# Kernel optimization log

Hardware: AMD Instinct MI355X
Metric: run time of the kernel (lower is better)

The kernel has to match this reference:

```python
import jax, jax.numpy as jnp
import numpy as np

E, D, H, B = 8, 64, 512, 32768  # n_experts, state_dim, hidden width, batch
IN = D + 3  # x, t, sin(omega*t), cos(omega*t)


def setup_inputs() -> dict:
    key = jax.random.key(0)
    ks = jax.random.split(key, 12)
    s = 0.02
    return {
        "t": jax.random.uniform(ks[0], (1,), dtype=jnp.float32),
        "x": jax.random.normal(ks[1], (B, D), dtype=jnp.float32),
        "expert_weights": jax.random.uniform(ks[2], (B, E), dtype=jnp.float32),
        "omega": jnp.arange(1, E + 1, dtype=jnp.float32),  # omega_i = i+1
        "W1": jax.random.normal(ks[3], (E, H, IN), dtype=jnp.float32) * s,
        "b1": jnp.zeros((E, H), dtype=jnp.float32),
        "W2": jax.random.normal(ks[4], (E, H, H), dtype=jnp.float32) * s,
        "b2": jnp.zeros((E, H), dtype=jnp.float32),
        "W3": jax.random.normal(ks[5], (E, H, H), dtype=jnp.float32) * s,
        "b3": jnp.zeros((E, H), dtype=jnp.float32),
        "W4": jax.random.normal(ks[6], (E, D, H), dtype=jnp.float32) * s,
        "b4": jnp.zeros((E, D), dtype=jnp.float32),
    }


def reference(t, x, expert_weights, omega, W1, b1, W2, b2, W3, b3, W4, b4):
    # Dense path of ExpertODEEnsemble.forward: all experts active.
    nB = x.shape[0]
    tb = jnp.broadcast_to(t, (nB,))                       # (B,)
    wt = omega[:, None] * tb[None, :]                     # (E, B)
    # Per-expert inputs: [x, t, sin(wt), cos(wt)] -> (E, B, D+3)
    xe = jnp.broadcast_to(x[None], (E, nB, D))
    te = jnp.broadcast_to(tb[None, :, None], (E, nB, 1))
    inp = jnp.concatenate([xe, te, jnp.sin(wt)[..., None], jnp.cos(wt)[..., None]], axis=-1)
    h = jnp.tanh(jnp.einsum('ebi,ehi->ebh', inp, W1) + b1[:, None, :])
    h = jnp.tanh(jnp.einsum('ebh,egh->ebg', h, W2) + b2[:, None, :])
    h = jnp.tanh(jnp.einsum('ebh,egh->ebg', h, W3) + b3[:, None, :])
    dyn = jnp.einsum('ebh,edh->ebd', h, W4) + b4[:, None, :]   # (E, B, D)
    # Weighted combine: sum_e w[b,e] * dyn[e,b,:]
    dx_dt = jnp.einsum('be,ebd->bd', expert_weights, dyn)
    return dx_dt
```

## Files before the change

### kernel.cpp

```cpp
#include <hip/hip_runtime.h>
#include <hip/hip_bf16.h>


typedef unsigned short ushort_t;
typedef unsigned int u32;
typedef unsigned long long u64;
typedef __attribute__((ext_vector_type(8))) short short8;
typedef __attribute__((ext_vector_type(4))) float floatx4;
typedef __attribute__((ext_vector_type(16))) float floatx16;
typedef __attribute__((ext_vector_type(4))) int intx4;

#define W1A_OFF 0u
#define W2A_OFF 524288u
#define W3A_OFF 4718592u
#define W4A_OFF 8912896u
#define XB_OFF  9437184u
#define B1E_OFF 13631488u

#define SLOTB 16384
#define X_OFF_L 131072
#define SYNC_OFF 147456
#define SMEM_SZ 147552

static __device__ __forceinline__ u32 pk2bf(float a, float b) {
  union { __hip_bfloat162 h; u32 u; } v;
  v.h = __float22bfloat162_rn(make_float2(a, b));
  return v.u;
}

static __device__ __forceinline__ float pade_tanh(float x) {
  float x2 = x * x;
  float num = __builtin_fmaf(x2, __builtin_fmaf(x2, 1.0f, 105.0f), 945.0f);
  float den = __builtin_fmaf(x2, __builtin_fmaf(x2, 15.0f, 420.0f), 945.0f);
  return x * num * __builtin_amdgcn_rcpf(den);
}

static __device__ __forceinline__ void ald16(const void* g, void* l) {
  __builtin_amdgcn_global_load_lds((__attribute__((address_space(1))) void*)g,
                                   (__attribute__((address_space(3))) void*)l,
                                   16, 0, 0);
}

static __device__ __forceinline__ floatx16 mfma32(short8 a, short8 b, floatx16 c) {
  return __builtin_amdgcn_mfma_f32_32x32x16_bf16(a, b, c, 0, 0, 0);
}

static __device__ __forceinline__ int slot8(int g, int b) {
  return ((g + b) & 7) * SLOTB;
}

static __device__ __forceinline__ void waitge(const int* p, int tgt) {
  while (*(volatile const int*)p < tgt) __builtin_amdgcn_s_sleep(1);
  __asm__ __volatile__("" ::: "memory");
}

static __device__ __forceinline__ void waitge4(const int* p, int tgt) {
  for (;;) {
    __asm__ __volatile__("" ::: "memory");
    intx4 v = *(const intx4*)p;
    if (v[0] >= tgt && v[1] >= tgt && v[2] >= tgt && v[3] >= tgt) break;
    __builtin_amdgcn_s_sleep(1);
  }
  __asm__ __volatile__("" ::: "memory");
}

static __device__ __forceinline__ void guard_grp(const int* grp, int w, int base) {
  int tg0 = base + ((0 - w - 1) & 7) + 1;
  int tg1 = base + ((1 - w - 1) & 7) + 1;
  int tg2 = base + ((2 - w - 1) & 7) + 1;
  int tg3 = base + ((3 - w - 1) & 7) + 1;
  int tg4 = base + ((4 - w - 1) & 7) + 1;
  int tg5 = base + ((5 - w - 1) & 7) + 1;
  int tg6 = base + ((6 - w - 1) & 7) + 1;
  int tg7 = base + ((7 - w - 1) & 7) + 1;
  for (;;) {
    __asm__ __volatile__("" ::: "memory");
    intx4 a = *(const intx4*)grp;
    intx4 b = *(const intx4*)(grp + 4);
    if (a[0] >= tg0 && a[1] >= tg1 && a[2] >= tg2 && a[3] >= tg3 &&
        b[0] >= tg4 && b[1] >= tg5 && b[2] >= tg6 && b[3] >= tg7) break;
    __builtin_amdgcn_s_sleep(1);
  }
  __asm__ __volatile__("" ::: "memory");
}

static __device__ __forceinline__ void bump(int* p, int lane) {
  __asm__ __volatile__("s_waitcnt lgkmcnt(0)" ::: "memory");
  if (lane == 0) atomicAdd(p, 1);
}

static __device__ __forceinline__ void bump_sig(int* p, int lane) {
  __builtin_amdgcn_sched_barrier(0);
  if (lane == 0) atomicAdd(p, 1);
}

__global__ __launch_bounds__(256) void prep_kernel(
    const float* __restrict__ t, const float* __restrict__ x,
    const float* __restrict__ omega, const float* __restrict__ W1,
    const float* __restrict__ b1, const float* __restrict__ W2,
    const float* __restrict__ W3, const float* __restrict__ W4,
    char* __restrict__ ws) {
  int i = blockIdx.x * 256 + threadIdx.x;
  if (i < 32768) {
    int e = i >> 12, d = i & 4095;
    int lane = d & 63, q = d >> 6;
    int ol = q & 1, kc = (q >> 1) & 3, w = q >> 3;
    int outr = w * 64 + ol * 32 + (lane & 31);
    int kg = kc * 2 + (lane >> 5);
    const float* s = W1 + (e * 512 + outr) * 67 + kg * 8;
    ((intx4*)(ws + W1A_OFF))[i] = (intx4){
        (int)pk2bf(s[0], s[1]), (int)pk2bf(s[2], s[3]),
        (int)pk2bf(s[4], s[5]), (int)pk2bf(s[6], s[7])};
    return;
  }
  i -= 32768;
  if (i < 262144) {
    int e = i >> 15, d = i & 32767;
    int lane = d & 63, q = d >> 6;
    int ol = q & 1, kc = (q >> 1) & 31, w = q >> 6;
    int outr = w * 64 + ol * 32 + (lane & 31);
    int kg = kc * 2 + (lane >> 5);
    const floatx4* s = (const floatx4*)(W2 + ((e << 9) + outr) * 512 + (kg << 3));
    floatx4 lo = s[0], hi = s[1];
    ((intx4*)(ws + W2A_OFF))[i] = (intx4){
        (int)pk2bf(lo[0], lo[1]), (int)pk2bf(lo[2], lo[3]),
        (int)pk2bf(hi[0], hi[1]), (int)pk2bf(hi[2], hi[3])};
    return;
  }
  i -= 262144;
  if (i < 262144) {
    int e = i >> 15, d = i & 32767;
    int lane = d & 63, q = d >> 6;
    int ol = q & 1, kc = (q >> 1) & 31, w = q >> 6;
    int outr = w * 64 + ol * 32 + (lane & 31);
    int kg = kc * 2 + (lane >> 5);
    const floatx4* s = (const floatx4*)(W3 + ((e << 9) + outr) * 512 + (kg << 3));
    floatx4 lo = s[0], hi = s[1];
    ((intx4*)(ws + W3A_OFF))[i] = (intx4){
        (int)pk2bf(lo[0], lo[1]), (int)pk2bf(lo[2], lo[3]),
        (int)pk2bf(hi[0], hi[1]), (int)pk2bf(hi[2], hi[3])};
    return;
  }
  i -= 262144;
  if (i < 32768) {
    int e = i >> 12, d = i & 4095;
    int lane = d & 63, q = d >> 6;
    int kc = q & 31, o4 = q >> 5;
    int outr = o4 * 32 + (lane & 31);
    int kg = kc * 2 + (lane >> 5);
    const floatx4* s = (const floatx4*)(W4 + ((e << 6) + outr) * 512 + (kg << 3));
    floatx4 lo = s[0], hi = s[1];
    ((intx4*)(ws + W4A_OFF))[i] = (intx4){
        (int)pk2bf(lo[0], lo[1]), (int)pk2bf(lo[2], lo[3]),
        (int)pk2bf(hi[0], hi[1]), (int)pk2bf(hi[2], hi[3])};
    return;
  }
  i -= 32768;
  if (i < 262144) {
    const floatx4* s = (const floatx4*)(x + i * 8);
    floatx4 lo = s[0], hi = s[1];
    ((intx4*)(ws + XB_OFF))[i] = (intx4){
        (int)pk2bf(lo[0], lo[1]), (int)pk2bf(lo[2], lo[3]),
        (int)pk2bf(hi[0], hi[1]), (int)pk2bf(hi[2], hi[3])};
    return;
  }
  i -= 262144;
  if (i < 4096) {
    float tv = t[0];
    int e = i >> 9;
    float om = omega[e];
    ((float*)(ws + B1E_OFF))[i] = b1[i] + tv * W1[i * 67 + 64]
        + sinf(om * tv) * W1[i * 67 + 65] + cosf(om * tv) * W1[i * 67 + 66];
  }
}


static __device__ __forceinline__ void epi_write(
    floatx16 acc[2][4], char* __restrict__ act, int wbyte, int r31, int q1) {
#pragma unroll
  for (int ol = 0; ol < 2; ++ol) {
#pragma unroll
    for (int g = 0; g < 4; ++g) {
      int ko = ol * 4 + g;
      char* base = act + wbyte + (ko >> 1) * 4096
                   + (((ko & 1) * 32 + r31) << 4) + q1 * 8;
#pragma unroll
      for (int nt = 0; nt < 4; ++nt) {
        float v0 = pade_tanh(acc[ol][nt][4 * g + 0]);
        float v1 = pade_tanh(acc[ol][nt][4 * g + 1]);
        float v2 = pade_tanh(acc[ol][nt][4 * g + 2]);
        float v3 = pade_tanh(acc[ol][nt][4 * g + 3]);
        u32 lo = pk2bf(v0, v1), hi = pk2bf(v2, v3);
        *(u64*)(base + nt * 1024) = ((u64)hi << 32) | lo;
      }
    }
  }
}

static __device__ __forceinline__ void mlp_l1(
    char* __restrict__ act, const char* __restrict__ xreg,
    int* pub, int* l4c, int lane, int w, int q1, int r31,
    const char* __restrict__ Abase, const float* __restrict__ bias,
    int wbyte, int e) {
  const int voff = lane * 16;
  const char* ap = Abase + w * 8192 + voff;

  floatx16 acc[2][4];
#pragma unroll
  for (int ol = 0; ol < 2; ++ol) {
    int fe0 = w * 64 + ol * 32 + 4 * q1;
#pragma unroll
    for (int g = 0; g < 4; ++g) {
      floatx4 bv = *(const floatx4*)(bias + fe0 + 8 * g);
#pragma unroll
      for (int nt = 0; nt < 4; ++nt) {
        acc[ol][nt][4 * g + 0] = bv[0];
        acc[ol][nt][4 * g + 1] = bv[1];
        acc[ol][nt][4 * g + 2] = bv[2];
        acc[ol][nt][4 * g + 3] = bv[3];
      }
    }
  }
  const char* xb0 = xreg + voff;
  short8 b0 = *(const short8*)(xb0);
  short8 b1v = *(const short8*)(xb0 + 1024);
  short8 b2 = *(const short8*)(xb0 + 2048);
  short8 b3 = *(const short8*)(xb0 + 3072);
  short8 a0 = *(const short8*)(ap);
  short8 a1 = *(const short8*)(ap + 1024);

#pragma unroll
  for (int j = 0; j < 4; ++j) {
    int jn = (j < 3) ? (j + 1) : 3;
    const char* xn = xreg + jn * 4096 + voff;
    const char* apn = (j < 3) ? (ap + 2048) : ap;
    short8 an0 = *(const short8*)(apn);
    short8 an1 = *(const short8*)(apn + 1024);
    short8 bn0 = *(const short8*)(xn);
    short8 bn1 = *(const short8*)(xn + 1024);
    short8 bn2 = *(const short8*)(xn + 2048);
    short8 bn3 = *(const short8*)(xn + 3072);
    __builtin_amdgcn_s_setprio(1);
    acc[0][0] = mfma32(a0, b0, acc[0][0]);
    acc[0][1] = mfma32(a0, b1v, acc[0][1]);
    acc[0][2] = mfma32(a0, b2, acc[0][2]);
    acc[0][3] = mfma32(a0, b3, acc[0][3]);
    acc[1][0] = mfma32(a1, b0, acc[1][0]);
    acc[1][1] = mfma32(a1, b1v, acc[1][1]);
    acc[1][2] = mfma32(a1, b2, acc[1][2]);
    acc[1][3] = mfma32(a1, b3, acc[1][3]);
    __builtin_amdgcn_s_setprio(0);
    a0 = an0; a1 = an1;
    b0 = bn0; b1v = bn1; b2 = bn2; b3 = bn3;
    ap = apn;
  }
  if (e > 0) waitge4(l4c + ((((w + 1) & 7) >> 2) << 2), e);
  epi_write(acc, act, wbyte, r31, q1);
  bump(pub + w, lane);
}

static __device__ __forceinline__ void mlp_mid(
    char* __restrict__ act, int* pub, int* grp, int lane, int w, int q1, int r31,
    const char* __restrict__ Abase, const float* __restrict__ bias,
    int pub_tgt, int rbase, int wbyte, int gbase) {
  const int voff = lane * 16;
  const char* spA = Abase + w * 65536 + voff;

  floatx16 acc[2][4];
#pragma unroll
  for (int ol = 0; ol < 2; ++ol) {
    int fe0 = w * 64 + ol * 32 + 4 * q1;
#pragma unroll
    for (int g = 0; g < 4; ++g) {
      floatx4 bv = *(const floatx4*)(bias + fe0 + 8 * g);
#pragma unroll
      for (int nt = 0; nt < 4; ++nt) {
        acc[ol][nt][4 * g + 0] = bv[0];
        acc[ol][nt][4 * g + 1] = bv[1];
        acc[ol][nt][4 * g + 2] = bv[2];
        acc[ol][nt][4 * g + 3] = bv[3];
      }
    }
  }
  const char* gb = act + slot8(w, rbase) + voff;
  const char* ap = spA + (4 * w) * 2048;
  short8 b0 = *(const short8*)(gb);
  short8 b1v = *(const short8*)(gb + 1024);
  short8 b2 = *(const short8*)(gb + 2048);
  short8 b3 = *(const short8*)(gb + 3072);
  short8 a0 = *(const short8*)(ap);
  short8 a1 = *(const short8*)(ap + 1024);

#pragma unroll 1
  for (int i = 0; i < 8; ++i) {
#pragma unroll
    for (int j = 0; j < 4; ++j) {
      const char* apn;
      const char* gbn = gb;
      const char* bsl;
      if (j < 3) {
        apn = ap + 2048;
        bsl = gb + (j + 1) * 4096;
      } else if (i < 7) {
        int g2 = (w - i - 1) & 7;
        waitge(pub + g2, pub_tgt);
        gbn = act + slot8(g2, rbase) + voff;
        apn = spA + (4 * g2) * 2048;
        bsl = gbn;
      } else {
        apn = ap; bsl = gb;
      }
      short8 an0 = *(const short8*)(apn);
      short8 an1 = *(const short8*)(apn + 1024);
      short8 bn0 = *(const short8*)(bsl);
      short8 bn1 = *(const short8*)(bsl + 1024);
      short8 bn2 = *(const short8*)(bsl + 2048);
      short8 bn3 = *(const short8*)(bsl + 3072);
      __builtin_amdgcn_s_setprio(1);
      acc[0][0] = mfma32(a0, b0, acc[0][0]);
      acc[0][1] = mfma32(a0, b1v, acc[0][1]);
      acc[0][2] = mfma32(a0, b2, acc[0][2]);
      acc[0][3] = mfma32(a0, b3, acc[0][3]);
      acc[1][0] = mfma32(a1, b0, acc[1][0]);
      acc[1][1] = mfma32(a1, b1v, acc[1][1]);
      acc[1][2] = mfma32(a1, b2, acc[1][2]);
      acc[1][3] = mfma32(a1, b3, acc[1][3]);
      __builtin_amdgcn_s_setprio(0);
      a0 = an0; a1 = an1;
      b0 = bn0; b1v = bn1; b2 = bn2; b3 = bn3;
      ap = apn; gb = gbn;
    }
    bump_sig(grp + w, lane);
  }

  guard_grp(grp, w, gbase);
  epi_write(acc, act, wbyte, r31, q1);
  bump(pub + w, lane);
}

extern "C" __global__ __launch_bounds__(512) void fused_kernel(
    const char* __restrict__ ws, const float* __restrict__ b2,
    const float* __restrict__ b3, const float* __restrict__ b4,
    const float* __restrict__ ew, float* __restrict__ out) {
  extern __shared__ char smem[];
  char* act = smem;
  char* xreg = smem + X_OFF_L;
  int* l4c = (int*)(smem + SYNC_OFF);
  int* pub = l4c + 8;
  int* grp = l4c + 16;

  const int t = threadIdx.x, lane = t & 63, w = t >> 6;
  const int q1 = lane >> 5, r31 = lane & 31;
  const int row0 = blockIdx.x << 7;
  const int voff = lane * 16;

  if (t < 24) ((int*)(smem + SYNC_OFF))[t] = 0;

  const ushort_t* xb = (const ushort_t*)(ws + XB_OFF);
#pragma unroll
  for (int s = 0; s < 2; ++s) {
    int u = w + 8 * s, v = u >> 2, nt = u & 3;
    ald16(xb + (row0 + nt * 32 + r31) * 64 + (2 * v + q1) * 8,
          xreg + v * 4096 + nt * 1024);
  }
  __syncthreads();

  for (int i = (7 - w) * 7; i > 0; --i) __builtin_amdgcn_s_sleep(1);

  const int rt = w & 3, kh = w >> 2;
  const int row_l4 = row0 + rt * 32 + r31;
  floatx16 oacc[2] = {};

  for (int e = 0; e < 8; ++e) {
    int b1s = (3 * e + 1) & 7;
    int b2s = (3 * e + 2) & 7;
    int b3s = (3 * e + 3) & 7;

    mlp_l1(act, xreg, pub, l4c, lane, w, q1, r31,
           (const char*)ws + W1A_OFF + e * 65536,
           (const float*)(ws + B1E_OFF) + e * 512, slot8(w, b1s), e);
    mlp_mid(act, pub, grp, lane, w, q1, r31,
            (const char*)ws + W2A_OFF + e * 524288, b2 + e * 512,
            3 * e + 1, b1s, slot8(w, b2s), 16 * e);
    mlp_mid(act, pub, grp, lane, w, q1, r31,
            (const char*)ws + W3A_OFF + e * 524288, b3 + e * 512,
            3 * e + 2, b2s, slot8(w, b3s), 16 * e + 8);

    {
      const char* spA4 = (const char*)ws + W4A_OFF + e * 65536 + voff;
      const float sc = ew[row_l4 * 8 + e];
      floatx16 acc4[2] = {};
      int g = 4 * kh + 3;
      waitge(pub + g, 3 * e + 3);
      const char* agb = spA4 + (4 * g) * 1024;
      const char* gb = act + slot8(g, b3s) + rt * 1024 + voff;
      short8 a0 = *(const short8*)(agb);
      short8 a1 = *(const short8*)(agb + 32768);
      short8 b = *(const short8*)(gb);
#pragma unroll 1
      for (int gl = 0; gl < 4; ++gl) {
#pragma unroll
        for (int j = 0; j < 4; ++j) {
          const char* agn = agb;
          const char* gbn = gb;
          const char* asl; const char* bsl;
          if (j < 3) {
            asl = agb + (j + 1) * 1024;
            bsl = gb + (j + 1) * 4096;
          } else if (gl < 3) {
            int g2 = g - 1;
            waitge(pub + g2, 3 * e + 3);
            agn = spA4 + (4 * g2) * 1024;
            gbn = act + slot8(g2, b3s) + rt * 1024 + voff;
            asl = agn; bsl = gbn;
          } else {
            asl = agb; bsl = gb;
          }
          short8 an0 = *(const short8*)(asl);
          short8 an1 = *(const short8*)(asl + 32768);
          short8 bn = *(const short8*)(bsl);
          __builtin_amdgcn_s_setprio(1);
          acc4[0] = mfma32(a0, b, acc4[0]);
          acc4[1] = mfma32(a1, b, acc4[1]);
          __builtin_amdgcn_s_setprio(0);
          a0 = an0; a1 = an1; b = bn;
          agb = agn; gb = gbn;
        }
        g = g - 1;
      }
      bump_sig(l4c + w, lane);
      if (kh == 0) {
        const float* bp = b4 + e * 64;
#pragma unroll
        for (int ol = 0; ol < 2; ++ol) {
          int fe0 = ol * 32 + 4 * q1;
#pragma unroll
          for (int g2 = 0; g2 < 4; ++g2) {
            floatx4 bv = *(const floatx4*)(bp + fe0 + 8 * g2);
            oacc[ol][4 * g2 + 0] += sc * (acc4[ol][4 * g2 + 0] + bv[0]);
            oacc[ol][4 * g2 + 1] += sc * (acc4[ol][4 * g2 + 1] + bv[1]);
            oacc[ol][4 * g2 + 2] += sc * (acc4[ol][4 * g2 + 2] + bv[2]);
            oacc[ol][4 * g2 + 3] += sc * (acc4[ol][4 * g2 + 3] + bv[3]);
          }
        }
      } else {
#pragma unroll
        for (int ol = 0; ol < 2; ++ol)
#pragma unroll
          for (int i = 0; i < 16; ++i) oacc[ol][i] += sc * acc4[ol][i];
      }
    }
  }

  __syncthreads();
  if (kh == 1) {
#pragma unroll
    for (int ol = 0; ol < 2; ++ol)
#pragma unroll
      for (int g = 0; g < 4; ++g) {
        floatx4 p = {oacc[ol][4 * g + 0], oacc[ol][4 * g + 1],
                     oacc[ol][4 * g + 2], oacc[ol][4 * g + 3]};
        *(floatx4*)(act + rt * 8192 + ol * 4096 + g * 1024 + lane * 16) = p;
      }
  }
  __syncthreads();
  if (kh == 0) {
    float* orow = out + (size_t)row_l4 * 64;
#pragma unroll
    for (int ol = 0; ol < 2; ++ol)
#pragma unroll
      for (int g = 0; g < 4; ++g) {
        floatx4 p = *(const floatx4*)(act + rt * 8192 + ol * 4096 + g * 1024 + lane * 16);
        floatx4 v = {oacc[ol][4 * g + 0] + p[0], oacc[ol][4 * g + 1] + p[1],
                     oacc[ol][4 * g + 2] + p[2], oacc[ol][4 * g + 3] + p[3]};
        *(floatx4*)(orow + ol * 32 + 8 * g + 4 * q1) = v;
      }
  }
}

extern "C" void kernel_launch(void* const* d_in, const int* in_sizes, int n_in,
                              void* d_out, int out_size, void* d_ws, size_t ws_size,
                              hipStream_t stream) {
  const float* t  = (const float*)d_in[0];
  const float* x  = (const float*)d_in[1];
  const float* ew = (const float*)d_in[2];
  const float* om = (const float*)d_in[3];
  const float* W1 = (const float*)d_in[4];
  const float* b1 = (const float*)d_in[5];
  const float* W2 = (const float*)d_in[6];
  const float* b2 = (const float*)d_in[7];
  const float* W3 = (const float*)d_in[8];
  const float* b3 = (const float*)d_in[9];
  const float* W4 = (const float*)d_in[10];
  const float* b4 = (const float*)d_in[11];
  char* ws = (char*)d_ws;
  float* out = (float*)d_out;
  (void)in_sizes; (void)n_in; (void)ws_size; (void)out_size;

  static int smem_set = 0;
  if (!smem_set) {
    hipFuncSetAttribute((const void*)fused_kernel,
                        hipFuncAttributeMaxDynamicSharedMemorySize, SMEM_SZ);
    smem_set = 1;
  }
  prep_kernel<<<3344, 256, 0, stream>>>(t, x, om, W1, b1, W2, W3, W4, ws);
  fused_kernel<<<256, 512, SMEM_SZ, stream>>>(ws, b2, b3, b4, ew, out);
}
```

Before: 427.2 us.

## Halve rows per block to 64 and accumulate output via global memory

Each block now handles 64 rows instead of 128, which halves the LDS footprint and the accumulator tiles, and sets launch_bounds(512,4) so more blocks can be resident per CU. The grid doubles to 512 blocks. The layer-4 output is no longer kept in registers and reduced through LDS at the end. Instead it is read, modified and written in global memory each expert, with flag handshakes between the two K-halves, and the staggered startup sleep is removed. The change gives up software prefetch of operands and per-block weight reuse in exchange for occupancy, and it adds global read-modify-write traffic and extra synchronisation.

```diff
diff --git a/kernel.cpp b/kernel.cpp
--- a/kernel.cpp
+++ b/kernel.cpp
@@ -17,10 +17,10 @@
 #define XB_OFF  9437184u
 #define B1E_OFF 13631488u
 
-#define SLOTB 16384
-#define X_OFF_L 131072
-#define SYNC_OFF 147456
-#define SMEM_SZ 147552
+#define SLOTB 8192
+#define X_OFF_L 65536
+#define SYNC_OFF 73728
+#define SMEM_SZ 73856
 
 static __device__ __forceinline__ u32 pk2bf(float a, float b) {
   union { __hip_bfloat162 h; u32 u; } v;
@@ -88,9 +88,12 @@
   __asm__ __volatile__("s_waitcnt lgkmcnt(0)" ::: "memory");
   if (lane == 0) atomicAdd(p, 1);
 }
-
 static __device__ __forceinline__ void bump_sig(int* p, int lane) {
   __builtin_amdgcn_sched_barrier(0);
+  if (lane == 0) atomicAdd(p, 1);
+}
+static __device__ __forceinline__ void bump_vm(int* p, int lane) {
+  __asm__ __volatile__("s_waitcnt vmcnt(0)" ::: "memory");
   if (lane == 0) atomicAdd(p, 1);
 }
 
@@ -175,17 +178,17 @@
 }
 
 
-static __device__ __forceinline__ void epi_write(
-    floatx16 acc[2][4], char* __restrict__ act, int wbyte, int r31, int q1) {
+static __device__ __forceinline__ void epi_write2(
+    floatx16 acc[2][2], char* __restrict__ act, int wbyte, int r31, int q1) {
 #pragma unroll
   for (int ol = 0; ol < 2; ++ol) {
 #pragma unroll
     for (int g = 0; g < 4; ++g) {
       int ko = ol * 4 + g;
-      char* base = act + wbyte + (ko >> 1) * 4096
+      char* base = act + wbyte + (ko >> 1) * 2048
                    + (((ko & 1) * 32 + r31) << 4) + q1 * 8;
 #pragma unroll
-      for (int nt = 0; nt < 4; ++nt) {
+      for (int nt = 0; nt < 2; ++nt) {
         float v0 = pade_tanh(acc[ol][nt][4 * g + 0]);
         float v1 = pade_tanh(acc[ol][nt][4 * g + 1]);
         float v2 = pade_tanh(acc[ol][nt][4 * g + 2]);
@@ -197,6 +200,45 @@
   }
 }
 
+static __device__ __forceinline__ void burst2(
+    floatx16 acc[2][2], const char* ap, const char* bp) {
+  short8 a00 = *(const short8*)(ap);
+  short8 a01 = *(const short8*)(ap + 1024);
+  short8 a10 = *(const short8*)(ap + 2048);
+  short8 a11 = *(const short8*)(ap + 3072);
+  short8 b00 = *(const short8*)(bp);
+  short8 b01 = *(const short8*)(bp + 1024);
+  short8 b10 = *(const short8*)(bp + 2048);
+  short8 b11 = *(const short8*)(bp + 3072);
+  acc[0][0] = mfma32(a00, b00, acc[0][0]);
+  acc[0][1] = mfma32(a00, b01, acc[0][1]);
+  acc[1][0] = mfma32(a01, b00, acc[1][0]);
+  acc[1][1] = mfma32(a01, b01, acc[1][1]);
+  acc[0][0] = mfma32(a10, b10, acc[0][0]);
+  acc[0][1] = mfma32(a10, b11, acc[0][1]);
+  acc[1][0] = mfma32(a11, b10, acc[1][0]);
+  acc[1][1] = mfma32(a11, b11, acc[1][1]);
+}
+
+static __device__ __forceinline__ void acc_init(
+    floatx16 acc[2][2], const float* bias, int w, int q1) {
+#pragma unroll
+  for (int ol = 0; ol < 2; ++ol) {
+    int fe0 = w * 64 + ol * 32 + 4 * q1;
+#pragma unroll
+    for (int g = 0; g < 4; ++g) {
+      floatx4 bv = *(const floatx4*)(bias + fe0 + 8 * g);
+#pragma unroll
+      for (int nt = 0; nt < 2; ++nt) {
+        acc[ol][nt][4 * g + 0] = bv[0];
+        acc[ol][nt][4 * g + 1] = bv[1];
+        acc[ol][nt][4 * g + 2] = bv[2];
+        acc[ol][nt][4 * g + 3] = bv[3];
+      }
+    }
+  }
+}
+
 static __device__ __forceinline__ void mlp_l1(
     char* __restrict__ act, const char* __restrict__ xreg,
     int* pub, int* l4c, int lane, int w, int q1, int r31,
@@ -204,58 +246,13 @@
     int wbyte, int e) {
   const int voff = lane * 16;
   const char* ap = Abase + w * 8192 + voff;
-
-  floatx16 acc[2][4];
-#pragma unroll
-  for (int ol = 0; ol < 2; ++ol) {
-    int fe0 = w * 64 + ol * 32 + 4 * q1;
-#pragma unroll
-    for (int g = 0; g < 4; ++g) {
-      floatx4 bv = *(const floatx4*)(bias + fe0 + 8 * g);
-#pragma unroll
-      for (int nt = 0; nt < 4; ++nt) {
-        acc[ol][nt][4 * g + 0] = bv[0];
-        acc[ol][nt][4 * g + 1] = bv[1];
-        acc[ol][nt][4 * g + 2] = bv[2];
-        acc[ol][nt][4 * g + 3] = bv[3];
-      }
-    }
-  }
-  const char* xb0 = xreg + voff;
-  short8 b0 = *(const short8*)(xb0);
-  short8 b1v = *(const short8*)(xb0 + 1024);
-  short8 b2 = *(const short8*)(xb0 + 2048);
-  short8 b3 = *(const short8*)(xb0 + 3072);
-  short8 a0 = *(const short8*)(ap);
-  short8 a1 = *(const short8*)(ap + 1024);
-
-#pragma unroll
-  for (int j = 0; j < 4; ++j) {
-    int jn = (j < 3) ? (j + 1) : 3;
-    const char* xn = xreg + jn * 4096 + voff;
-    const char* apn = (j < 3) ? (ap + 2048) : ap;
-    short8 an0 = *(const short8*)(apn);
-    short8 an1 = *(const short8*)(apn + 1024);
-    short8 bn0 = *(const short8*)(xn);
-    short8 bn1 = *(const short8*)(xn + 1024);
-    short8 bn2 = *(const short8*)(xn + 2048);
-    short8 bn3 = *(const short8*)(xn + 3072);
-    __builtin_amdgcn_s_setprio(1);
-    acc[0][0] = mfma32(a0, b0, acc[0][0]);
-    acc[0][1] = mfma32(a0, b1v, acc[0][1]);
-    acc[0][2] = mfma32(a0, b2, acc[0][2]);
-    acc[0][3] = mfma32(a0, b3, acc[0][3]);
-    acc[1][0] = mfma32(a1, b0, acc[1][0]);
-    acc[1][1] = mfma32(a1, b1v, acc[1][1]);
-    acc[1][2] = mfma32(a1, b2, acc[1][2]);
-    acc[1][3] = mfma32(a1, b3, acc[1][3]);
-    __builtin_amdgcn_s_setprio(0);
-    a0 = an0; a1 = an1;
-    b0 = bn0; b1v = bn1; b2 = bn2; b3 = bn3;
-    ap = apn;
-  }
+  floatx16 acc[2][2];
+  acc_init(acc, bias, w, q1);
+#pragma unroll
+  for (int js = 0; js < 2; ++js)
+    burst2(acc, ap + js * 4096, xreg + js * 4096 + voff);
   if (e > 0) waitge4(l4c + ((((w + 1) & 7) >> 2) << 2), e);
-  epi_write(acc, act, wbyte, r31, q1);
+  epi_write2(acc, act, wbyte, r31, q1);
   bump(pub + w, lane);
 }
 
@@ -265,80 +262,25 @@
     int pub_tgt, int rbase, int wbyte, int gbase) {
   const int voff = lane * 16;
   const char* spA = Abase + w * 65536 + voff;
-
-  floatx16 acc[2][4];
-#pragma unroll
-  for (int ol = 0; ol < 2; ++ol) {
-    int fe0 = w * 64 + ol * 32 + 4 * q1;
-#pragma unroll
-    for (int g = 0; g < 4; ++g) {
-      floatx4 bv = *(const floatx4*)(bias + fe0 + 8 * g);
-#pragma unroll
-      for (int nt = 0; nt < 4; ++nt) {
-        acc[ol][nt][4 * g + 0] = bv[0];
-        acc[ol][nt][4 * g + 1] = bv[1];
-        acc[ol][nt][4 * g + 2] = bv[2];
-        acc[ol][nt][4 * g + 3] = bv[3];
-      }
-    }
-  }
-  const char* gb = act + slot8(w, rbase) + voff;
-  const char* ap = spA + (4 * w) * 2048;
-  short8 b0 = *(const short8*)(gb);
-  short8 b1v = *(const short8*)(gb + 1024);
-  short8 b2 = *(const short8*)(gb + 2048);
-  short8 b3 = *(const short8*)(gb + 3072);
-  short8 a0 = *(const short8*)(ap);
-  short8 a1 = *(const short8*)(ap + 1024);
-
+  floatx16 acc[2][2];
+  acc_init(acc, bias, w, q1);
 #pragma unroll 1
   for (int i = 0; i < 8; ++i) {
-#pragma unroll
-    for (int j = 0; j < 4; ++j) {
-      const char* apn;
-      const char* gbn = gb;
-      const char* bsl;
-      if (j < 3) {
-        apn = ap + 2048;
-        bsl = gb + (j + 1) * 4096;
-      } else if (i < 7) {
-        int g2 = (w - i - 1) & 7;
-        waitge(pub + g2, pub_tgt);
-        gbn = act + slot8(g2, rbase) + voff;
-        apn = spA + (4 * g2) * 2048;
-        bsl = gbn;
-      } else {
-        apn = ap; bsl = gb;
-      }
-      short8 an0 = *(const short8*)(apn);
-      short8 an1 = *(const short8*)(apn + 1024);
-      short8 bn0 = *(const short8*)(bsl);
-      short8 bn1 = *(const short8*)(bsl + 1024);
-      short8 bn2 = *(const short8*)(bsl + 2048);
-      short8 bn3 = *(const short8*)(bsl + 3072);
-      __builtin_amdgcn_s_setprio(1);
-      acc[0][0] = mfma32(a0, b0, acc[0][0]);
-      acc[0][1] = mfma32(a0, b1v, acc[0][1]);
-      acc[0][2] = mfma32(a0, b2, acc[0][2]);
-      acc[0][3] = mfma32(a0, b3, acc[0][3]);
-      acc[1][0] = mfma32(a1, b0, acc[1][0]);
-      acc[1][1] = mfma32(a1, b1v, acc[1][1]);
-      acc[1][2] = mfma32(a1, b2, acc[1][2]);
-      acc[1][3] = mfma32(a1, b3, acc[1][3]);
-      __builtin_amdgcn_s_setprio(0);
-      a0 = an0; a1 = an1;
-      b0 = bn0; b1v = bn1; b2 = bn2; b3 = bn3;
-      ap = apn; gb = gbn;
-    }
+    int g = (w - i) & 7;
+    if (i > 0) waitge(pub + g, pub_tgt);
+    const char* gb = act + slot8(g, rbase) + voff;
+    const char* ap = spA + g * 8192;
+#pragma unroll
+    for (int js = 0; js < 2; ++js)
+      burst2(acc, ap + js * 4096, gb + js * 4096);
     bump_sig(grp + w, lane);
   }
-
   guard_grp(grp, w, gbase);
-  epi_write(acc, act, wbyte, r31, q1);
+  epi_write2(acc, act, wbyte, r31, q1);
   bump(pub + w, lane);
 }
 
-extern "C" __global__ __launch_bounds__(512) void fused_kernel(
+extern "C" __global__ __launch_bounds__(512, 4) void fused_kernel(
     const char* __restrict__ ws, const float* __restrict__ b2,
     const float* __restrict__ b3, const float* __restrict__ b4,
     const float* __restrict__ ew, float* __restrict__ out) {
@@ -348,28 +290,26 @@
   int* l4c = (int*)(smem + SYNC_OFF);
   int* pub = l4c + 8;
   int* grp = l4c + 16;
+  int* okh0 = l4c + 24;
+  int* okh1 = l4c + 28;
 
   const int t = threadIdx.x, lane = t & 63, w = t >> 6;
   const int q1 = lane >> 5, r31 = lane & 31;
-  const int row0 = blockIdx.x << 7;
+  const int row0 = blockIdx.x << 6;
   const int voff = lane * 16;
 
-  if (t < 24) ((int*)(smem + SYNC_OFF))[t] = 0;
-
-  const ushort_t* xb = (const ushort_t*)(ws + XB_OFF);
-#pragma unroll
-  for (int s = 0; s < 2; ++s) {
-    int u = w + 8 * s, v = u >> 2, nt = u & 3;
+  if (t < 32) ((int*)(smem + SYNC_OFF))[t] = 0;
+
+  {
+    const ushort_t* xb = (const ushort_t*)(ws + XB_OFF);
+    int v = w >> 1, nt = w & 1;
     ald16(xb + (row0 + nt * 32 + r31) * 64 + (2 * v + q1) * 8,
-          xreg + v * 4096 + nt * 1024);
+          xreg + v * 2048 + nt * 1024);
   }
   __syncthreads();
 
-  for (int i = (7 - w) * 7; i > 0; --i) __builtin_amdgcn_s_sleep(1);
-
-  const int rt = w & 3, kh = w >> 2;
-  const int row_l4 = row0 + rt * 32 + r31;
-  floatx16 oacc[2] = {};
+  const int o4 = w & 1, nt4 = (w >> 1) & 1, kh = w >> 2, pp = w & 3;
+  const int row_l4 = row0 + nt4 * 32 + r31;
 
   for (int e = 0; e < 8; ++e) {
     int b1s = (3 * e + 1) & 7;
@@ -387,94 +327,56 @@
             3 * e + 2, b2s, slot8(w, b3s), 16 * e + 8);
 
     {
-      const char* spA4 = (const char*)ws + W4A_OFF + e * 65536 + voff;
-      const float sc = ew[row_l4 * 8 + e];
-      floatx16 acc4[2] = {};
-      int g = 4 * kh + 3;
-      waitge(pub + g, 3 * e + 3);
-      const char* agb = spA4 + (4 * g) * 1024;
-      const char* gb = act + slot8(g, b3s) + rt * 1024 + voff;
-      short8 a0 = *(const short8*)(agb);
-      short8 a1 = *(const short8*)(agb + 32768);
-      short8 b = *(const short8*)(gb);
+      const char* apW4 = (const char*)ws + W4A_OFF + e * 65536
+                         + o4 * 32768 + voff;
+      floatx16 acc4 = {};
 #pragma unroll 1
       for (int gl = 0; gl < 4; ++gl) {
-#pragma unroll
-        for (int j = 0; j < 4; ++j) {
-          const char* agn = agb;
-          const char* gbn = gb;
-          const char* asl; const char* bsl;
-          if (j < 3) {
-            asl = agb + (j + 1) * 1024;
-            bsl = gb + (j + 1) * 4096;
-          } else if (gl < 3) {
-            int g2 = g - 1;
-            waitge(pub + g2, 3 * e + 3);
-            agn = spA4 + (4 * g2) * 1024;
-            gbn = act + slot8(g2, b3s) + rt * 1024 + voff;
-            asl = agn; bsl = gbn;
-          } else {
-            asl = agb; bsl = gb;
-          }
-          short8 an0 = *(const short8*)(asl);
-          short8 an1 = *(const short8*)(asl + 32768);
-          short8 bn = *(const short8*)(bsl);
-          __builtin_amdgcn_s_setprio(1);
-          acc4[0] = mfma32(a0, b, acc4[0]);
-          acc4[1] = mfma32(a1, b, acc4[1]);
-          __builtin_amdgcn_s_setprio(0);
-          a0 = an0; a1 = an1; b = bn;
-          agb = agn; gb = gbn;
+        int g = 4 * kh + gl;
+        waitge(pub + g, 3 * e + 3);
+        const char* gb = act + slot8(g, b3s) + nt4 * 1024 + voff;
+#pragma unroll
+        for (int s = 0; s < 4; ++s) {
+          short8 a = *(const short8*)(apW4 + (4 * g + s) * 1024);
+          short8 b = *(const short8*)(gb + s * 2048);
+          acc4 = mfma32(a, b, acc4);
         }
-        g = g - 1;
       }
       bump_sig(l4c + w, lane);
+
+      const float sc = ew[row_l4 * 8 + e];
+      float* orow = out + (size_t)row_l4 * 64 + o4 * 32;
       if (kh == 0) {
-        const float* bp = b4 + e * 64;
-#pragma unroll
-        for (int ol = 0; ol < 2; ++ol) {
-          int fe0 = ol * 32 + 4 * q1;
-#pragma unroll
-          for (int g2 = 0; g2 < 4; ++g2) {
-            floatx4 bv = *(const floatx4*)(bp + fe0 + 8 * g2);
-            oacc[ol][4 * g2 + 0] += sc * (acc4[ol][4 * g2 + 0] + bv[0]);
-            oacc[ol][4 * g2 + 1] += sc * (acc4[ol][4 * g2 + 1] + bv[1]);
-            oacc[ol][4 * g2 + 2] += sc * (acc4[ol][4 * g2 + 2] + bv[2]);
-            oacc[ol][4 * g2 + 3] += sc * (acc4[ol][4 * g2 + 3] + bv[3]);
-          }
+        if (e > 0) waitge(okh1 + pp, e);
+        const float* bp = b4 + e * 64 + o4 * 32;
+#pragma unroll
+        for (int g2 = 0; g2 < 4; ++g2) {
+          floatx4 bv = *(const floatx4*)(bp + 8 * g2 + 4 * q1);
+          float* dst = orow + 8 * g2 + 4 * q1;
+          floatx4 cur = (e > 0) ? *(const floatx4*)dst
+                                : (floatx4){0.f, 0.f, 0.f, 0.f};
+          floatx4 v = {cur[0] + sc * (acc4[4 * g2 + 0] + bv[0]),
+                       cur[1] + sc * (acc4[4 * g2 + 1] + bv[1]),
+                       cur[2] + sc * (acc4[4 * g2 + 2] + bv[2]),
+                       cur[3] + sc * (acc4[4 * g2 + 3] + bv[3])};
+          *(floatx4*)dst = v;
         }
+        bump_vm(okh0 + pp, lane);
       } else {
-#pragma unroll
-        for (int ol = 0; ol < 2; ++ol)
-#pragma unroll
-          for (int i = 0; i < 16; ++i) oacc[ol][i] += sc * acc4[ol][i];
+        waitge(okh0 + pp, e + 1);
+#pragma unroll
+        for (int g2 = 0; g2 < 4; ++g2) {
+          float* dst = orow + 8 * g2 + 4 * q1;
+          floatx4 cur = *(const floatx4*)dst;
+          floatx4 v = {cur[0] + sc * acc4[4 * g2 + 0],
+                       cur[1] + sc * acc4[4 * g2 + 1],
+                       cur[2] + sc * acc4[4 * g2 + 2],
+                       cur[3] + sc * acc4[4 * g2 + 3]};
+          *(floatx4*)dst = v;
+        }
+        bump_vm(okh1 + pp, lane);
       }
     }
-  }
-
-  __syncthreads();
-  if (kh == 1) {
-#pragma unroll
-    for (int ol = 0; ol < 2; ++ol)
-#pragma unroll
-      for (int g = 0; g < 4; ++g) {
-        floatx4 p = {oacc[ol][4 * g + 0], oacc[ol][4 * g + 1],
-                     oacc[ol][4 * g + 2], oacc[ol][4 * g + 3]};
-        *(floatx4*)(act + rt * 8192 + ol * 4096 + g * 1024 + lane * 16) = p;
-      }
-  }
-  __syncthreads();
-  if (kh == 0) {
-    float* orow = out + (size_t)row_l4 * 64;
-#pragma unroll
-    for (int ol = 0; ol < 2; ++ol)
-#pragma unroll
-      for (int g = 0; g < 4; ++g) {
-        floatx4 p = *(const floatx4*)(act + rt * 8192 + ol * 4096 + g * 1024 + lane * 16);
-        floatx4 v = {oacc[ol][4 * g + 0] + p[0], oacc[ol][4 * g + 1] + p[1],
-                     oacc[ol][4 * g + 2] + p[2], oacc[ol][4 * g + 3] + p[3]};
-        *(floatx4*)(orow + ol * 32 + 8 * g + 4 * q1) = v;
-      }
   }
 }
 
@@ -504,5 +406,5 @@
     smem_set = 1;
   }
   prep_kernel<<<3344, 256, 0, stream>>>(t, x, om, W1, b1, W2, W3, W4, ws);
-  fused_kernel<<<256, 512, SMEM_SZ, stream>>>(ws, b2, b3, b4, ew, out);
-}
+  fused_kernel<<<512, 512, SMEM_SZ, stream>>>(ws, b2, b3, b4, ew, out);
+}
```

Measured after the change: 492.4 us. +15.3%, slower.
